# Kernel tuning notes

Hardware: AMD Instinct MI355X
Metric: run time of the kernel (lower is better)

Reference implementation:

```python
import jax, jax.numpy as jnp
import numpy as np

DIM = 768
NUM_HEADS = 12
HEAD_DIM = DIM // NUM_HEADS
GRID = 32  # H == W
EPS = 1e-6


def setup_inputs() -> dict:
    key = jax.random.key(0)
    ks = jax.random.split(key, 8)
    B, N = 8, GRID * GRID
    x = jax.random.normal(ks[0], (B, N, DIM), dtype=jnp.float32)
    policy = jax.random.randint(ks[1], (B, N, 1), 0, 2).astype(jnp.float32)
    qkv_w = jax.random.normal(ks[2], (3 * DIM, DIM), dtype=jnp.float32) * 0.02
    qkv_b = jax.random.normal(ks[3], (3 * DIM,), dtype=jnp.float32) * 0.02
    proj_w = jax.random.normal(ks[4], (DIM, DIM), dtype=jnp.float32) * 0.02
    proj_b = jax.random.normal(ks[5], (DIM,), dtype=jnp.float32) * 0.02
    rel_pos_h = jax.random.normal(ks[6], (2 * GRID - 1, HEAD_DIM), dtype=jnp.float32) * 0.02
    rel_pos_w = jax.random.normal(ks[7], (2 * GRID - 1, HEAD_DIM), dtype=jnp.float32) * 0.02
    return {"x": x, "policy": policy, "qkv_w": qkv_w, "qkv_b": qkv_b,
            "proj_w": proj_w, "proj_b": proj_b,
            "rel_pos_h": rel_pos_h, "rel_pos_w": rel_pos_w, "H": GRID, "W": GRID}


def _attention(x, policy, qkv_w, qkv_b, proj_w, proj_b, rel_pos_h, rel_pos_w, H, W):
    B, N, C = x.shape
    nh, hd = NUM_HEADS, C // NUM_HEADS
    scale = hd ** (-0.5)
    # qkv projection: [B,N,3C] -> [3, B*nh, N, hd]
    qkv = (x @ qkv_w.T + qkv_b).reshape(B, N, 3, nh, hd)
    qkv = qkv.transpose(2, 0, 3, 1, 4).reshape(3, B * nh, N, hd)
    q, k, v = qkv[0], qkv[1], qkv[2]
    attn = jnp.einsum("bqd,bkd->bqk", q * scale, k)  # [B*nh, N, N]
    # decomposed relative position bias (q_size == k_size == (H, W))
    coords = jnp.arange(H)
    Rh = rel_pos_h[coords[:, None] - coords[None, :] + (H - 1)]  # [H,H,hd]
    coords_w = jnp.arange(W)
    Rw = rel_pos_w[coords_w[:, None] - coords_w[None, :] + (W - 1)]  # [W,W,hd]
    r_q = q.reshape(B * nh, H, W, hd)
    rel_h = jnp.einsum("bhwc,hkc->bhwk", r_q, Rh)  # [B*nh,H,W,H]
    rel_w = jnp.einsum("bhwc,wkc->bhwk", r_q, Rw)  # [B*nh,H,W,W]
    attn = (attn.reshape(B * nh, H, W, H, W)
            + rel_h[:, :, :, :, None]
            + rel_w[:, :, :, None, :]).reshape(B * nh, N, N)
    # policy-masked softmax
    attn = attn.reshape(B, nh, N, N)
    ap = policy.reshape(B, 1, 1, N)
    ap = ap + (1.0 - ap) * jnp.eye(N, dtype=ap.dtype)  # always attend to self
    max_att = jnp.max(attn, axis=-1, keepdims=True)
    e = jnp.exp(attn - max_att).astype(jnp.float32) * ap.astype(jnp.float32)
    attn = ((e + EPS / N) / (jnp.sum(e, axis=-1, keepdims=True) + EPS)).astype(x.dtype)
    out = jnp.einsum("bqk,bkd->bqd", attn.reshape(B * nh, N, N), v)
    out = out.reshape(B, nh, N, hd).transpose(0, 2, 1, 3).reshape(B, N, C)
    return out @ proj_w.T + proj_b


def reference(x, policy, qkv_w, qkv_b, proj_w, proj_b, rel_pos_h, rel_pos_w, H, W):
    return _attention(x, policy, qkv_w, qkv_b, proj_w, proj_b, rel_pos_h, rel_pos_w, H, W)
```

## Files before the change

### kernel.cpp

```cpp
#include <hip/hip_runtime.h>
#include <hip/hip_bf16.h>

#define B_   8
#define N_   1024
#define C_   768
#define NH_  12
#define HD_  64
#define BH_  96
#define EPS_ 1e-6f
#define EPSN_ (1e-6f / 1024.0f)
#define SQ_  0.1803368801111244f

typedef __bf16 bf16;
typedef __attribute__((ext_vector_type(8))) __bf16  bf16x8;
typedef __attribute__((ext_vector_type(4))) __bf16  bf16x4;
typedef __attribute__((ext_vector_type(4))) float   floatx4;

#define MFMA16(a, b, c) __builtin_amdgcn_mfma_f32_16x16x32_bf16((a), (b), (c), 0, 0, 0)

__device__ __forceinline__ void gld16(const void* g, void* l) {
  typedef unsigned int u32;
  __builtin_amdgcn_global_load_lds(
      (const __attribute__((address_space(1))) u32*)g,
      (__attribute__((address_space(3))) u32*)l, 16, 0, 0);
}
__device__ __forceinline__ float bfu2f(unsigned int u) {
  union { unsigned int i; float f; } v; v.i = u << 16; return v.f;
}
__device__ __forceinline__ float bfhi2f(unsigned int u) {
  union { unsigned int i; float f; } v; v.i = u & 0xffff0000u; return v.f;
}
__device__ __forceinline__ unsigned short f2bfu(float f) {
  union { float f; unsigned int i; } v; v.f = f;
  return (unsigned short)((v.i + 0x7FFFu + ((v.i >> 16) & 1u)) >> 16);
}

__global__ __launch_bounds__(256) void prep_kernel(
    const float* __restrict__ x, const float* __restrict__ qkv_w,
    const float* __restrict__ proj_w, const float* __restrict__ relh,
    const float* __restrict__ relw,
    bf16* __restrict__ Xb, bf16* __restrict__ Wq, bf16* __restrict__ Wp,
    bf16* __restrict__ Rhb, bf16* __restrict__ Rwb) {
  int bid = blockIdx.x;
  if (bid < 8448) {
    const float* in; bf16* out; int i;
    if (bid < 6144)      { in = x;      out = Xb; i = bid * 256 + threadIdx.x; }
    else if (bid < 7872) { in = qkv_w;  out = Wq; i = (bid - 6144) * 256 + threadIdx.x; }
    else                 { in = proj_w; out = Wp; i = (bid - 7872) * 256 + threadIdx.x; }
    float4 v = ((const float4*)in)[i];
    bf16x4 o = {(bf16)v.x, (bf16)v.y, (bf16)v.z, (bf16)v.w};
    ((bf16x4*)out)[i] = o;
  } else {
    const float* in = (bid < 8464) ? relh : relw;
    bf16* out = (bid < 8464) ? Rhb : Rwb;
    int i = ((bid < 8464) ? (bid - 8448) : (bid - 8464)) * 256 + threadIdx.x;
    int r = i >> 6;
    out[i] = (r < 63) ? (bf16)(in[i] * 8.0f) : (bf16)0.0f;
  }
}

__global__ __launch_bounds__(256) void gemm_qkv(
    const bf16* __restrict__ X, const bf16* __restrict__ W,
    const float* __restrict__ bias,
    bf16* __restrict__ Qb, bf16* __restrict__ Kb, bf16* __restrict__ Vb) {
  __shared__ __align__(16) bf16 As[128 * 64];
  __shared__ __align__(16) bf16 Bs[128 * 64];
  const int tid = threadIdx.x;
  const int lane = tid & 63, quad = lane >> 4, c16 = lane & 15;
  const int wid = tid >> 6;
  const int wm = (wid >> 1) * 64, wn = (wid & 1) * 64;
  const int m0 = blockIdx.x * 128, n0 = blockIdx.y * 128;
  const bool flip = (blockIdx.y < 12);
  floatx4 acc[4][4];
#pragma unroll
  for (int i = 0; i < 4; ++i)
#pragma unroll
    for (int j = 0; j < 4; ++j) acc[i][j] = {0.f, 0.f, 0.f, 0.f};

  for (int k0 = 0; k0 < 768; k0 += 64) {
    __syncthreads();
#pragma unroll
    for (int t = 0; t < 4; ++t) {
      int task = t * 256 + tid;
      int r = task >> 3, lg = (task & 7) ^ (r & 7);
      int wbase = (t * 256 + (tid & 192)) * 8;
      gld16(X + (size_t)(m0 + r) * 768 + k0 + lg * 8, &As[wbase]);
      gld16(W + (size_t)(n0 + r) * 768 + k0 + lg * 8, &Bs[wbase]);
    }
    __syncthreads();
#pragma unroll
    for (int kw = 0; kw < 2; ++kw) {
      bf16x8 af[4], bfr[4];
#pragma unroll
      for (int i = 0; i < 4; ++i) {
        int r = wm + i * 16 + c16, pg = (kw * 4 + quad) ^ (c16 & 7);
        af[i] = *(bf16x8*)&As[r * 64 + pg * 8];
      }
#pragma unroll
      for (int j = 0; j < 4; ++j) {
        int r = wn + j * 16 + c16, pg = (kw * 4 + quad) ^ (c16 & 7);
        bfr[j] = *(bf16x8*)&Bs[r * 64 + pg * 8];
      }
      if (flip) {
#pragma unroll
        for (int a = 0; a < 4; ++a)
#pragma unroll
          for (int b = 0; b < 4; ++b) acc[a][b] = MFMA16(bfr[a], af[b], acc[a][b]);
      } else {
#pragma unroll
        for (int i = 0; i < 4; ++i)
#pragma unroll
          for (int j = 0; j < 4; ++j) acc[i][j] = MFMA16(af[i], bfr[j], acc[i][j]);
      }
    }
  }
  if (flip) {
    const bool isQ = (blockIdx.y < 6);
    bf16* base = isQ ? Qb : Kb;
    const int off = isQ ? 0 : 768;
#pragma unroll
    for (int a = 0; a < 4; ++a) {
      int jb = n0 + wn + a * 16 + quad * 4;
      float4 b4 = *(const float4*)&bias[jb];
      int head = (jb - off) >> 6;
      int d = jb & 63;
#pragma unroll
      for (int b = 0; b < 4; ++b) {
        int tok = m0 + wm + b * 16 + c16;
        int bb = tok >> 10, n = tok & 1023;
        float v0 = acc[a][b][0] + b4.x, v1 = acc[a][b][1] + b4.y;
        float v2 = acc[a][b][2] + b4.z, v3 = acc[a][b][3] + b4.w;
        if (isQ) { v0 *= SQ_; v1 *= SQ_; v2 *= SQ_; v3 *= SQ_; }
        bf16x4 o = {(bf16)v0, (bf16)v1, (bf16)v2, (bf16)v3};
        *(bf16x4*)&base[(((size_t)bb * NH_ + head) * N_ + n) * HD_ + d] = o;
      }
    }
  } else {
#pragma unroll
    for (int jt = 0; jt < 4; ++jt) {
      int j = n0 + wn + jt * 16 + c16;
      float bj = bias[j];
      int rem = j - 1536, head = rem >> 6, d = rem & 63;
#pragma unroll
      for (int it = 0; it < 4; ++it) {
        int mbase = m0 + wm + it * 16 + quad * 4;
        int bb = mbase >> 10, n = mbase & 1023;
        bf16x4 o = {(bf16)(acc[it][jt][0] + bj), (bf16)(acc[it][jt][1] + bj),
                    (bf16)(acc[it][jt][2] + bj), (bf16)(acc[it][jt][3] + bj)};
        *(bf16x4*)&Vb[(((size_t)bb * NH_ + head) * HD_ + d) * N_ + n] = o;
      }
    }
  }
}

__global__ __launch_bounds__(256) void vsum_kernel(const bf16* __restrict__ Vb,
                                                   float* __restrict__ Vsum) {
  const int bh = blockIdx.x;
  const int d = threadIdx.x >> 2, part = threadIdx.x & 3;
  const bf16* Vg = Vb + (size_t)bh * (N_ * HD_) + d * N_ + part * 256;
  float s = 0.f;
  for (int i = 0; i < 32; ++i) {
    bf16x8 v = *(const bf16x8*)(Vg + i * 8);
#pragma unroll
    for (int e = 0; e < 8; ++e) s += (float)v[e];
  }
  __shared__ float red[64][4];
  red[d][part] = s;
  __syncthreads();
  if (part == 0) Vsum[bh * 64 + d] = red[d][0] + red[d][1] + red[d][2] + red[d][3];
}

__global__ __launch_bounds__(256, 4) void attn_mfma(
    const bf16* __restrict__ Qb, const bf16* __restrict__ Kb,
    const bf16* __restrict__ Vb, const float* __restrict__ policy,
    const bf16* __restrict__ Rh, const bf16* __restrict__ Rw,
    const float* __restrict__ Vsum, bf16* __restrict__ AO) {
  const int bh = blockIdx.x, qt = blockIdx.y;
  const int b = bh / NH_, head = bh % NH_;
  __shared__ __align__(16) bf16 Qs[4096];
  __shared__ __align__(16) bf16 Ks[4096];
  __shared__ __align__(16) bf16 Vt[4096];
  __shared__ unsigned short RHb[64][34];
  __shared__ unsigned short RWb[64][34];
  __shared__ float polf[1024];
  const int tid = threadIdx.x;
  const int wid = tid >> 6, lane = tid & 63, quad = lane >> 4, c16 = lane & 15;
  const int sw = c16 & 7;
  bf16* Ptw = Qs + wid * 1024;
  const floatx4 zero4 = {0.f, 0.f, 0.f, 0.f};

  const bf16* Qg = Qb + ((size_t)bh * N_ + qt * 64) * HD_;
  const bf16* Kg = Kb + (size_t)bh * (N_ * HD_);
  const bf16* Vg = Vb + (size_t)bh * (N_ * HD_);

#pragma unroll
  for (int t = 0; t < 2; ++t) {
    int task = t * 256 + tid;
    int r = task >> 3, lg = (task & 7) ^ (r & 7);
    int wbase = (t * 256 + (tid & 192)) * 8;
    gld16(Qg + r * 64 + lg * 8, &Qs[wbase]);
    gld16(Rh + r * 64 + lg * 8, &Ks[wbase]);
  }
  gld16(policy + (size_t)b * N_ + tid * 4, &polf[(tid & 192) * 4]);
  __syncthreads();

  bf16x8 aq0 = *(bf16x8*)&Qs[(wid * 16 + c16) * 64 + (quad ^ sw) * 8];
  bf16x8 aq1 = *(bf16x8*)&Qs[(wid * 16 + c16) * 64 + ((4 + quad) ^ sw) * 8];

  {
    floatx4 racc[4];
#pragma unroll
    for (int nt = 0; nt < 4; ++nt) {
      int r = nt * 16 + c16;
      bf16x8 b0 = *(bf16x8*)&Ks[r * 64 + (quad ^ sw) * 8];
      bf16x8 b1 = *(bf16x8*)&Ks[r * 64 + ((4 + quad) ^ sw) * 8];
      racc[nt] = MFMA16(aq1, b1, MFMA16(aq0, b0, zero4));
    }
#pragma unroll
    for (int nt = 0; nt < 4; ++nt)
#pragma unroll
      for (int reg = 0; reg < 4; ++reg) {
        int rloc = wid * 16 + quad * 4 + reg;
        int hh = 2 * qt + (rloc >> 5);
        int krow = hh + 31 - (nt * 16 + c16);
        if ((unsigned)krow < 32u) RHb[rloc][krow] = f2bfu(racc[nt][reg]);
      }
  }
  __syncthreads();
#pragma unroll
  for (int t = 0; t < 2; ++t) {
    int task = t * 256 + tid;
    int r = task >> 3, lg = (task & 7) ^ (r & 7);
    gld16(Rw + r * 64 + lg * 8, &Ks[(t * 256 + (tid & 192)) * 8]);
  }
  __syncthreads();
  {
    floatx4 racc[4];
#pragma unroll
    for (int nt = 0; nt < 4; ++nt) {
      int r = nt * 16 + c16;
      bf16x8 b0 = *(bf16x8*)&Ks[r * 64 + (quad ^ sw) * 8];
      bf16x8 b1 = *(bf16x8*)&Ks[r * 64 + ((4 + quad) ^ sw) * 8];
      racc[nt] = MFMA16(aq1, b1, MFMA16(aq0, b0, zero4));
    }
#pragma unroll
    for (int nt = 0; nt < 4; ++nt)
#pragma unroll
      for (int reg = 0; reg < 4; ++reg) {
        int rloc = wid * 16 + quad * 4 + reg;
        int kcol = (rloc & 31) + 31 - (nt * 16 + c16);
        if ((unsigned)kcol < 32u) RWb[rloc][kcol] = f2bfu(racc[nt][reg]);
      }
  }

  float rwv0[4], rwv1[4];
#pragma unroll
  for (int reg = 0; reg < 4; ++reg) {
    int rloc = wid * 16 + quad * 4 + reg;
    rwv0[reg] = bfu2f(RWb[rloc][c16]);
    rwv1[reg] = bfu2f(RWb[rloc][16 + c16]);
  }
  int ptoff[4][4];
#pragma unroll
  for (int reg = 0; reg < 4; ++reg) {
    int prow = quad * 4 + reg;
#pragma unroll
    for (int nt = 0; nt < 4; ++nt)
      ptoff[reg][nt] = prow * 64 + (c16 & 7) +
                       (((nt * 2 + (c16 >> 3)) ^ (prow & 7)) << 3);
  }

  float l_part[4] = {0.f, 0.f, 0.f, 0.f};
  floatx4 o_acc[4];
#pragma unroll
  for (int i = 0; i < 4; ++i) o_acc[i] = zero4;
  int nqr[4];
#pragma unroll
  for (int reg = 0; reg < 4; ++reg) nqr[reg] = qt * 64 + wid * 16 + quad * 4 + reg;

  for (int kt = 0; kt < 16; ++kt) {
    __syncthreads();
#pragma unroll
    for (int t = 0; t < 2; ++t) {
      int task = t * 256 + tid;
      int r = task >> 3, lg = (task & 7) ^ (r & 7);
      int wbase = (t * 256 + (tid & 192)) * 8;
      gld16(Kg + (size_t)(kt * 64 + r) * 64 + lg * 8, &Ks[wbase]);
      gld16(Vg + (size_t)r * N_ + kt * 64 + lg * 8, &Vt[wbase]);
    }

    floatx4 init[4];
#pragma unroll
    for (int reg = 0; reg < 4; ++reg) {
      int rloc = wid * 16 + quad * 4 + reg;
      unsigned int rhp = *(const unsigned int*)&RHb[rloc][kt * 2];
      float rh0 = bfu2f(rhp & 0xffffu), rh1 = bfhi2f(rhp);
      init[0][reg] = rh0 + rwv0[reg];
      init[1][reg] = rh0 + rwv1[reg];
      init[2][reg] = rh1 + rwv0[reg];
      init[3][reg] = rh1 + rwv1[reg];
    }
    float pm[4];
#pragma unroll
    for (int nt = 0; nt < 4; ++nt) pm[nt] = polf[kt * 64 + nt * 16 + c16];
    __syncthreads();

    floatx4 s[4];
#pragma unroll
    for (int nt = 0; nt < 4; ++nt) {
      int r = nt * 16 + c16;
      bf16x8 bk0 = *(bf16x8*)&Ks[r * 64 + (quad ^ sw) * 8];
      bf16x8 bk1 = *(bf16x8*)&Ks[r * 64 + ((4 + quad) ^ sw) * 8];
      s[nt] = MFMA16(aq1, bk1, MFMA16(aq0, bk0, init[nt]));
    }

#pragma unroll
    for (int reg = 0; reg < 4; ++reg) {
      if (kt != qt) {
#pragma unroll
        for (int nt = 0; nt < 4; ++nt) {
          float e = exp2f(s[nt][reg]) * pm[nt];
          l_part[reg] += e;
          Ptw[ptoff[reg][nt]] = (bf16)e;
        }
      } else {
        const int nq = nqr[reg];
#pragma unroll
        for (int nt = 0; nt < 4; ++nt) {
          int kg = kt * 64 + nt * 16 + c16;
          float mask = (kg == nq) ? 1.f : pm[nt];
          float e = exp2f(s[nt][reg]) * mask;
          l_part[reg] += e;
          Ptw[ptoff[reg][nt]] = (bf16)e;
        }
      }
    }

#pragma unroll
    for (int kw2 = 0; kw2 < 2; ++kw2) {
      bf16x8 ap = *(bf16x8*)&Ptw[c16 * 64 + ((kw2 * 4 + quad) ^ sw) * 8];
#pragma unroll
      for (int dt = 0; dt < 4; ++dt) {
        int r = dt * 16 + c16;
        bf16x8 bv = *(bf16x8*)&Vt[r * 64 + ((kw2 * 4 + quad) ^ sw) * 8];
        o_acc[dt] = MFMA16(ap, bv, o_acc[dt]);
      }
    }
  }

  float inv[4];
#pragma unroll
  for (int reg = 0; reg < 4; ++reg) {
    float l = l_part[reg];
#pragma unroll
    for (int d = 1; d < 16; d <<= 1) l += __shfl_xor(l, d, 64);
    inv[reg] = 1.f / (l + EPS_);
  }
#pragma unroll
  for (int dt = 0; dt < 4; ++dt) {
    int d = dt * 16 + c16;
    float vs = Vsum[bh * 64 + d];
#pragma unroll
    for (int reg = 0; reg < 4; ++reg) {
      float o = (o_acc[dt][reg] + EPSN_ * vs) * inv[reg];
      AO[((size_t)b * N_ + nqr[reg]) * C_ + head * HD_ + d] = (bf16)o;
    }
  }
}

__global__ __launch_bounds__(256) void gemm_proj(
    const bf16* __restrict__ A, const bf16* __restrict__ W,
    const float* __restrict__ bias, float* __restrict__ Out) {
  __shared__ __align__(16) bf16 As[128 * 64];
  __shared__ __align__(16) bf16 Bs[128 * 64];
  const int tid = threadIdx.x;
  const int lane = tid & 63, quad = lane >> 4, c16 = lane & 15;
  const int wid = tid >> 6;
  const int wm = (wid >> 1) * 64, wn = (wid & 1) * 64;
  const int m0 = blockIdx.x * 128, n0 = blockIdx.y * 128;
  floatx4 acc[4][4];
#pragma unroll
  for (int i = 0; i < 4; ++i)
#pragma unroll
    for (int j = 0; j < 4; ++j) acc[i][j] = {0.f, 0.f, 0.f, 0.f};

  for (int k0 = 0; k0 < 768; k0 += 64) {
    __syncthreads();
#pragma unroll
    for (int t = 0; t < 4; ++t) {
      int task = t * 256 + tid;
      int r = task >> 3, lg = (task & 7) ^ (r & 7);
      int wbase = (t * 256 + (tid & 192)) * 8;
      gld16(A + (size_t)(m0 + r) * 768 + k0 + lg * 8, &As[wbase]);
      gld16(W + (size_t)(n0 + r) * 768 + k0 + lg * 8, &Bs[wbase]);
    }
    __syncthreads();
#pragma unroll
    for (int kw = 0; kw < 2; ++kw) {
      bf16x8 af[4], bfr[4];
#pragma unroll
      for (int i = 0; i < 4; ++i) {
        int r = wm + i * 16 + c16, pg = (kw * 4 + quad) ^ (c16 & 7);
        af[i] = *(bf16x8*)&As[r * 64 + pg * 8];
      }
#pragma unroll
      for (int j = 0; j < 4; ++j) {
        int r = wn + j * 16 + c16, pg = (kw * 4 + quad) ^ (c16 & 7);
        bfr[j] = *(bf16x8*)&Bs[r * 64 + pg * 8];
      }
#pragma unroll
      for (int a = 0; a < 4; ++a)
#pragma unroll
        for (int b = 0; b < 4; ++b) acc[a][b] = MFMA16(bfr[a], af[b], acc[a][b]);
    }
  }
#pragma unroll
  for (int a = 0; a < 4; ++a) {
    int jb = n0 + wn + a * 16 + quad * 4;
    float4 b4 = *(const float4*)&bias[jb];
#pragma unroll
    for (int b = 0; b < 4; ++b) {
      int m = m0 + wm + b * 16 + c16;
      float4 o = make_float4(acc[a][b][0] + b4.x, acc[a][b][1] + b4.y,
                             acc[a][b][2] + b4.z, acc[a][b][3] + b4.w);
      *(float4*)&Out[(size_t)m * 768 + jb] = o;
    }
  }
}

extern "C" void kernel_launch(void* const* d_in, const int* in_sizes, int n_in,
                              void* d_out, int out_size, void* d_ws, size_t ws_size,
                              hipStream_t stream) {
  const float* x      = (const float*)d_in[0];
  const float* policy = (const float*)d_in[1];
  const float* qkv_w  = (const float*)d_in[2];
  const float* qkv_b  = (const float*)d_in[3];
  const float* proj_w = (const float*)d_in[4];
  const float* proj_b = (const float*)d_in[5];
  const float* relh   = (const float*)d_in[6];
  const float* relw   = (const float*)d_in[7];

  char* ws = (char*)d_ws;
  bf16* Xbf   = (bf16*)(ws);
  bf16* Wqkv  = (bf16*)(ws + 12582912);
  bf16* Wproj = (bf16*)(ws + 16121856);
  bf16* Rhb   = (bf16*)(ws + 17301504);
  bf16* Rwb   = (bf16*)(ws + 17309696);
  bf16* Qb    = (bf16*)(ws + 17317888);
  bf16* Kb    = (bf16*)(ws + 29900800);
  bf16* Vb    = (bf16*)(ws + 42483712);
  bf16* AOb   = (bf16*)(ws + 55066624);
  float* Vsum = (float*)(ws + 67649536);

  prep_kernel<<<8480, 256, 0, stream>>>(x, qkv_w, proj_w, relh, relw,
                                        Xbf, Wqkv, Wproj, Rhb, Rwb);
  gemm_qkv<<<dim3(64, 18), 256, 0, stream>>>(Xbf, Wqkv, qkv_b, Qb, Kb, Vb);
  vsum_kernel<<<BH_, 256, 0, stream>>>(Vb, Vsum);
  attn_mfma<<<dim3(BH_, 16), 256, 0, stream>>>(Qb, Kb, Vb, policy, Rhb, Rwb,
                                               Vsum, AOb);
  gemm_proj<<<dim3(64, 6), 256, 0, stream>>>(AOb, Wproj, proj_b, (float*)d_out);
}
```

Measured before the change: 234.5 us.

## Fuse V column sums into QKV GEMM and enlarge attention tile to 128 queries

The V column sums (used for the epsilon term) are now reduced in the QKV GEMM epilogue with wave shuffles and atomics, which removes the separate vsum kernel and its re-read of V. A memset zeroes the sums first. The attention kernel now uses 512-thread blocks covering 128 query rows, so each K/V tile load serves twice as many queries. The score MFMA is transposed so each lane holds four consecutive keys for one query, which allows vectorised policy loads, packed P stores and a cheaper row-sum reduction. In exchange the block uses more LDS and grid occupancy halves, and the atomics make summation order nondeterministic.

```diff
diff --git a/kernel.cpp b/kernel.cpp
--- a/kernel.cpp
+++ b/kernel.cpp
@@ -62,7 +62,8 @@
 __global__ __launch_bounds__(256) void gemm_qkv(
     const bf16* __restrict__ X, const bf16* __restrict__ W,
     const float* __restrict__ bias,
-    bf16* __restrict__ Qb, bf16* __restrict__ Kb, bf16* __restrict__ Vb) {
+    bf16* __restrict__ Qb, bf16* __restrict__ Kb, bf16* __restrict__ Vb,
+    float* __restrict__ Vsum) {
   __shared__ __align__(16) bf16 As[128 * 64];
   __shared__ __align__(16) bf16 Bs[128 * 64];
   const int tid = threadIdx.x;
@@ -136,52 +137,41 @@
       }
     }
   } else {
+    const int bb = (m0 + wm) >> 10;
 #pragma unroll
     for (int jt = 0; jt < 4; ++jt) {
       int j = n0 + wn + jt * 16 + c16;
       float bj = bias[j];
       int rem = j - 1536, head = rem >> 6, d = rem & 63;
+      float colsum = 16.0f * bj;
 #pragma unroll
       for (int it = 0; it < 4; ++it) {
         int mbase = m0 + wm + it * 16 + quad * 4;
-        int bb = mbase >> 10, n = mbase & 1023;
+        int n = mbase & 1023;
         bf16x4 o = {(bf16)(acc[it][jt][0] + bj), (bf16)(acc[it][jt][1] + bj),
                     (bf16)(acc[it][jt][2] + bj), (bf16)(acc[it][jt][3] + bj)};
         *(bf16x4*)&Vb[(((size_t)bb * NH_ + head) * HD_ + d) * N_ + n] = o;
-      }
-    }
-  }
-}
-
-__global__ __launch_bounds__(256) void vsum_kernel(const bf16* __restrict__ Vb,
-                                                   float* __restrict__ Vsum) {
-  const int bh = blockIdx.x;
-  const int d = threadIdx.x >> 2, part = threadIdx.x & 3;
-  const bf16* Vg = Vb + (size_t)bh * (N_ * HD_) + d * N_ + part * 256;
-  float s = 0.f;
-  for (int i = 0; i < 32; ++i) {
-    bf16x8 v = *(const bf16x8*)(Vg + i * 8);
-#pragma unroll
-    for (int e = 0; e < 8; ++e) s += (float)v[e];
-  }
-  __shared__ float red[64][4];
-  red[d][part] = s;
-  __syncthreads();
-  if (part == 0) Vsum[bh * 64 + d] = red[d][0] + red[d][1] + red[d][2] + red[d][3];
-}
-
-__global__ __launch_bounds__(256, 4) void attn_mfma(
+        colsum += acc[it][jt][0] + acc[it][jt][1] + acc[it][jt][2] + acc[it][jt][3];
+      }
+      colsum += __shfl_xor(colsum, 16, 64);
+      colsum += __shfl_xor(colsum, 32, 64);
+      if (quad == 0) atomicAdd(&Vsum[(bb * NH_ + head) * HD_ + d], colsum);
+    }
+  }
+}
+
+__global__ __launch_bounds__(512, 4) void attn_mfma(
     const bf16* __restrict__ Qb, const bf16* __restrict__ Kb,
     const bf16* __restrict__ Vb, const float* __restrict__ policy,
     const bf16* __restrict__ Rh, const bf16* __restrict__ Rw,
     const float* __restrict__ Vsum, bf16* __restrict__ AO) {
   const int bh = blockIdx.x, qt = blockIdx.y;
   const int b = bh / NH_, head = bh % NH_;
-  __shared__ __align__(16) bf16 Qs[4096];
+  __shared__ __align__(16) bf16 Qs[8192];
   __shared__ __align__(16) bf16 Ks[4096];
   __shared__ __align__(16) bf16 Vt[4096];
-  __shared__ unsigned short RHb[64][34];
-  __shared__ unsigned short RWb[64][34];
+  __shared__ unsigned short RHb[128][34];
+  __shared__ unsigned short RWb[128][34];
   __shared__ float polf[1024];
   const int tid = threadIdx.x;
   const int wid = tid >> 6, lane = tid & 63, quad = lane >> 4, c16 = lane & 15;
@@ -189,19 +179,21 @@
   bf16* Ptw = Qs + wid * 1024;
   const floatx4 zero4 = {0.f, 0.f, 0.f, 0.f};
 
-  const bf16* Qg = Qb + ((size_t)bh * N_ + qt * 64) * HD_;
+  const bf16* Qg = Qb + ((size_t)bh * N_ + qt * 128) * HD_;
   const bf16* Kg = Kb + (size_t)bh * (N_ * HD_);
   const bf16* Vg = Vb + (size_t)bh * (N_ * HD_);
 
 #pragma unroll
   for (int t = 0; t < 2; ++t) {
-    int task = t * 256 + tid;
+    int task = t * 512 + tid;
     int r = task >> 3, lg = (task & 7) ^ (r & 7);
-    int wbase = (t * 256 + (tid & 192)) * 8;
-    gld16(Qg + r * 64 + lg * 8, &Qs[wbase]);
-    gld16(Rh + r * 64 + lg * 8, &Ks[wbase]);
-  }
-  gld16(policy + (size_t)b * N_ + tid * 4, &polf[(tid & 192) * 4]);
+    gld16(Qg + r * 64 + lg * 8, &Qs[(t * 512 + (tid & 448)) * 8]);
+  }
+  {
+    int r = tid >> 3, lg = (tid & 7) ^ (r & 7);
+    gld16(Rh + r * 64 + lg * 8, &Ks[(tid & 448) * 8]);
+  }
+  if (tid < 256) gld16(policy + (size_t)b * N_ + tid * 4, &polf[(tid & 192) * 4]);
   __syncthreads();
 
   bf16x8 aq0 = *(bf16x8*)&Qs[(wid * 16 + c16) * 64 + (quad ^ sw) * 8];
@@ -221,17 +213,15 @@
 #pragma unroll
       for (int reg = 0; reg < 4; ++reg) {
         int rloc = wid * 16 + quad * 4 + reg;
-        int hh = 2 * qt + (rloc >> 5);
+        int hh = qt * 4 + (rloc >> 5);
         int krow = hh + 31 - (nt * 16 + c16);
         if ((unsigned)krow < 32u) RHb[rloc][krow] = f2bfu(racc[nt][reg]);
       }
   }
   __syncthreads();
-#pragma unroll
-  for (int t = 0; t < 2; ++t) {
-    int task = t * 256 + tid;
-    int r = task >> 3, lg = (task & 7) ^ (r & 7);
-    gld16(Rw + r * 64 + lg * 8, &Ks[(t * 256 + (tid & 192)) * 8]);
+  {
+    int r = tid >> 3, lg = (tid & 7) ^ (r & 7);
+    gld16(Rw + r * 64 + lg * 8, &Ks[(tid & 448) * 8]);
   }
   __syncthreads();
   {
@@ -253,87 +243,67 @@
       }
   }
 
-  float rwv0[4], rwv1[4];
-#pragma unroll
-  for (int reg = 0; reg < 4; ++reg) {
-    int rloc = wid * 16 + quad * 4 + reg;
-    rwv0[reg] = bfu2f(RWb[rloc][c16]);
-    rwv1[reg] = bfu2f(RWb[rloc][16 + c16]);
-  }
-  int ptoff[4][4];
-#pragma unroll
-  for (int reg = 0; reg < 4; ++reg) {
-    int prow = quad * 4 + reg;
-#pragma unroll
-    for (int nt = 0; nt < 4; ++nt)
-      ptoff[reg][nt] = prow * 64 + (c16 & 7) +
-                       (((nt * 2 + (c16 >> 3)) ^ (prow & 7)) << 3);
-  }
-
-  float l_part[4] = {0.f, 0.f, 0.f, 0.f};
+  const int qloc = wid * 16 + c16;
+  float rwv[2][4];
+#pragma unroll
+  for (int p = 0; p < 2; ++p)
+#pragma unroll
+    for (int reg = 0; reg < 4; ++reg)
+      rwv[p][reg] = bfu2f(RWb[qloc][p * 16 + quad * 4 + reg]);
+  int ptoff[4];
+#pragma unroll
+  for (int nt = 0; nt < 4; ++nt)
+    ptoff[nt] = c16 * 64 + (((nt * 2 + (quad >> 1)) ^ sw) << 3) + ((quad & 1) << 2);
+  const int ktq = qt * 2 + (wid >> 2);
+  const int kdiag = (wid & 3) * 16 + c16;
+
+  float l_lane = 0.f;
   floatx4 o_acc[4];
 #pragma unroll
   for (int i = 0; i < 4; ++i) o_acc[i] = zero4;
-  int nqr[4];
-#pragma unroll
-  for (int reg = 0; reg < 4; ++reg) nqr[reg] = qt * 64 + wid * 16 + quad * 4 + reg;
 
   for (int kt = 0; kt < 16; ++kt) {
     __syncthreads();
-#pragma unroll
-    for (int t = 0; t < 2; ++t) {
-      int task = t * 256 + tid;
-      int r = task >> 3, lg = (task & 7) ^ (r & 7);
-      int wbase = (t * 256 + (tid & 192)) * 8;
+    {
+      int r = tid >> 3, lg = (tid & 7) ^ (r & 7);
+      int wbase = (tid & 448) * 8;
       gld16(Kg + (size_t)(kt * 64 + r) * 64 + lg * 8, &Ks[wbase]);
       gld16(Vg + (size_t)r * N_ + kt * 64 + lg * 8, &Vt[wbase]);
     }
-
-    floatx4 init[4];
-#pragma unroll
-    for (int reg = 0; reg < 4; ++reg) {
-      int rloc = wid * 16 + quad * 4 + reg;
-      unsigned int rhp = *(const unsigned int*)&RHb[rloc][kt * 2];
-      float rh0 = bfu2f(rhp & 0xffffu), rh1 = bfhi2f(rhp);
-      init[0][reg] = rh0 + rwv0[reg];
-      init[1][reg] = rh0 + rwv1[reg];
-      init[2][reg] = rh1 + rwv0[reg];
-      init[3][reg] = rh1 + rwv1[reg];
-    }
-    float pm[4];
-#pragma unroll
-    for (int nt = 0; nt < 4; ++nt) pm[nt] = polf[kt * 64 + nt * 16 + c16];
-    __syncthreads();
-
-    floatx4 s[4];
+    unsigned int rhp = *(const unsigned int*)&RHb[qloc][kt * 2];
+    float rh0 = bfu2f(rhp & 0xffffu), rh1 = bfhi2f(rhp);
+    __syncthreads();
+
+    floatx4 st[4];
 #pragma unroll
     for (int nt = 0; nt < 4; ++nt) {
       int r = nt * 16 + c16;
       bf16x8 bk0 = *(bf16x8*)&Ks[r * 64 + (quad ^ sw) * 8];
       bf16x8 bk1 = *(bf16x8*)&Ks[r * 64 + ((4 + quad) ^ sw) * 8];
-      s[nt] = MFMA16(aq1, bk1, MFMA16(aq0, bk0, init[nt]));
-    }
-
-#pragma unroll
-    for (int reg = 0; reg < 4; ++reg) {
-      if (kt != qt) {
-#pragma unroll
-        for (int nt = 0; nt < 4; ++nt) {
-          float e = exp2f(s[nt][reg]) * pm[nt];
-          l_part[reg] += e;
-          Ptw[ptoff[reg][nt]] = (bf16)e;
-        }
+      floatx4 ci;
+      float rh = (nt < 2) ? rh0 : rh1;
+#pragma unroll
+      for (int reg = 0; reg < 4; ++reg) ci[reg] = rh + rwv[nt & 1][reg];
+      st[nt] = MFMA16(bk1, aq1, MFMA16(bk0, aq0, ci));
+    }
+
+#pragma unroll
+    for (int nt = 0; nt < 4; ++nt) {
+      float4 pm = *(const float4*)&polf[kt * 64 + nt * 16 + quad * 4];
+      float e0, e1, e2, e3;
+      if (kt != ktq) {
+        e0 = exp2f(st[nt][0]) * pm.x; e1 = exp2f(st[nt][1]) * pm.y;
+        e2 = exp2f(st[nt][2]) * pm.z; e3 = exp2f(st[nt][3]) * pm.w;
       } else {
-        const int nq = nqr[reg];
-#pragma unroll
-        for (int nt = 0; nt < 4; ++nt) {
-          int kg = kt * 64 + nt * 16 + c16;
-          float mask = (kg == nq) ? 1.f : pm[nt];
-          float e = exp2f(s[nt][reg]) * mask;
-          l_part[reg] += e;
-          Ptw[ptoff[reg][nt]] = (bf16)e;
-        }
-      }
+        int kb = nt * 16 + quad * 4;
+        e0 = exp2f(st[nt][0]) * ((kb + 0 == kdiag) ? 1.f : pm.x);
+        e1 = exp2f(st[nt][1]) * ((kb + 1 == kdiag) ? 1.f : pm.y);
+        e2 = exp2f(st[nt][2]) * ((kb + 2 == kdiag) ? 1.f : pm.z);
+        e3 = exp2f(st[nt][3]) * ((kb + 3 == kdiag) ? 1.f : pm.w);
+      }
+      l_lane += (e0 + e1) + (e2 + e3);
+      bf16x4 pe = {(bf16)e0, (bf16)e1, (bf16)e2, (bf16)e3};
+      *(bf16x4*)&Ptw[ptoff[nt]] = pe;
     }
 
 #pragma unroll
@@ -348,22 +318,23 @@
     }
   }
 
+  float l = l_lane;
+  l += __shfl_xor(l, 16, 64);
+  l += __shfl_xor(l, 32, 64);
+  float invl = 1.f / (l + EPS_);
   float inv[4];
 #pragma unroll
-  for (int reg = 0; reg < 4; ++reg) {
-    float l = l_part[reg];
-#pragma unroll
-    for (int d = 1; d < 16; d <<= 1) l += __shfl_xor(l, d, 64);
-    inv[reg] = 1.f / (l + EPS_);
-  }
+  for (int reg = 0; reg < 4; ++reg) inv[reg] = __shfl(invl, quad * 4 + reg, 64);
+
 #pragma unroll
   for (int dt = 0; dt < 4; ++dt) {
     int d = dt * 16 + c16;
     float vs = Vsum[bh * 64 + d];
 #pragma unroll
     for (int reg = 0; reg < 4; ++reg) {
+      int nq = qt * 128 + wid * 16 + quad * 4 + reg;
       float o = (o_acc[dt][reg] + EPSN_ * vs) * inv[reg];
-      AO[((size_t)b * N_ + nqr[reg]) * C_ + head * HD_ + d] = (bf16)o;
+      AO[((size_t)b * N_ + nq) * C_ + head * HD_ + d] = (bf16)o;
     }
   }
 }
@@ -452,11 +423,11 @@
   bf16* AOb   = (bf16*)(ws + 55066624);
   float* Vsum = (float*)(ws + 67649536);
 
+  hipMemsetAsync(Vsum, 0, BH_ * HD_ * sizeof(float), stream);
   prep_kernel<<<8480, 256, 0, stream>>>(x, qkv_w, proj_w, relh, relw,
                                         Xbf, Wqkv, Wproj, Rhb, Rwb);
-  gemm_qkv<<<dim3(64, 18), 256, 0, stream>>>(Xbf, Wqkv, qkv_b, Qb, Kb, Vb);
-  vsum_kernel<<<BH_, 256, 0, stream>>>(Vb, Vsum);
-  attn_mfma<<<dim3(BH_, 16), 256, 0, stream>>>(Qb, Kb, Vb, policy, Rhb, Rwb,
-                                               Vsum, AOb);
+  gemm_qkv<<<dim3(64, 18), 256, 0, stream>>>(Xbf, Wqkv, qkv_b, Qb, Kb, Vb, Vsum);
+  attn_mfma<<<dim3(BH_, 8), 512, 0, stream>>>(Qb, Kb, Vb, policy, Rhb, Rwb,
+                                              Vsum, AOb);
   gemm_proj<<<dim3(64, 6), 256, 0, stream>>>(AOb, Wproj, proj_b, (float*)d_out);
 }
```

Result: slower. 271.9 us (+15.9%).
